# Performance work log

Measured on AMD Instinct MI355X. Metric: run time of the kernel, lower is better.

Reference implementation:

```python
import jax, jax.numpy as jnp
import numpy as np
from jax import lax

T, B = 128, 256          # rollout length x num envs
H, W, C = 7, 7, 3        # minigrid obs
HID = 128                # lstm hidden
NA = 7                   # actions
NFLAT = 64 * 4 * 4       # conv flatten (7->6->5->4)


def setup_inputs() -> dict:
    key = jax.random.key(0)
    ks = jax.random.split(key, 20)
    N = T * B
    obs = jax.random.randint(ks[0], (N, H, W, C), 0, 11).astype(jnp.float32)
    done = (jax.random.uniform(ks[1], (N,)) < 0.05).astype(jnp.float32)
    h0 = jnp.zeros((1, B, HID), jnp.float32)
    c0 = jnp.zeros((1, B, HID), jnp.float32)
    s = 0.1
    conv1_w = jax.random.normal(ks[2], (16, C, 2, 2)) * s
    conv1_b = jnp.zeros((16,), jnp.float32)
    conv2_w = jax.random.normal(ks[3], (32, 16, 2, 2)) * s
    conv2_b = jnp.zeros((32,), jnp.float32)
    conv3_w = jax.random.normal(ks[4], (64, 32, 2, 2)) * s
    conv3_b = jnp.zeros((64,), jnp.float32)
    w_ih = jax.random.normal(ks[5], (4 * HID, NFLAT)) * 0.03
    w_hh = jax.random.normal(ks[6], (4 * HID, HID)) * 0.08
    b_ih = jnp.zeros((4 * HID,), jnp.float32)
    b_hh = jnp.zeros((4 * HID,), jnp.float32)
    actor_w = jax.random.normal(ks[7], (NA, HID)) * 0.01
    actor_b = jnp.zeros((NA,), jnp.float32)
    critic_w = jax.random.normal(ks[8], (1, HID)) * 0.08
    critic_b = jnp.zeros((1,), jnp.float32)
    return dict(obs=obs, done=done, h0=h0, c0=c0,
                conv1_w=conv1_w, conv1_b=conv1_b,
                conv2_w=conv2_w, conv2_b=conv2_b,
                conv3_w=conv3_w, conv3_b=conv3_b,
                w_ih=w_ih, w_hh=w_hh, b_ih=b_ih, b_hh=b_hh,
                actor_w=actor_w, actor_b=actor_b,
                critic_w=critic_w, critic_b=critic_b)


def _conv(x, w, b):
    # x: [N, Cin, h, w], w: [Cout, Cin, 2, 2], VALID, stride 1
    y = lax.conv_general_dilated(x, w, (1, 1), 'VALID',
                                 dimension_numbers=('NCHW', 'OIHW', 'NCHW'))
    return jax.nn.relu(y + b[None, :, None, None])


def reference(obs, done, h0, c0,
              conv1_w, conv1_b, conv2_w, conv2_b, conv3_w, conv3_b,
              w_ih, w_hh, b_ih, b_hh, actor_w, actor_b, critic_w, critic_b):
    N = obs.shape[0]
    x = jnp.transpose(obs, (0, 3, 1, 2))            # NHWC -> NCHW
    x = _conv(x, conv1_w, conv1_b)
    x = _conv(x, conv2_w, conv2_b)
    x = _conv(x, conv3_w, conv3_b)
    feat = x.reshape(N, -1)                          # [T*B, 1024]

    nb = h0.shape[1]
    xs = feat.reshape(-1, nb, feat.shape[-1])        # [T, B, 1024]
    ds = done.reshape(-1, nb)                        # [T, B]
    bias = b_ih + b_hh

    def step(carry, inp):
        h, c = carry                                  # [B, HID]
        x_t, d_t = inp
        m = (1.0 - d_t)[:, None]
        h = m * h
        c = m * c
        gates = x_t @ w_ih.T + h @ w_hh.T + bias      # [B, 4*HID]
        i, f, g, o = jnp.split(gates, 4, axis=-1)     # torch gate order i,f,g,o
        i = jax.nn.sigmoid(i)
        f = jax.nn.sigmoid(f)
        g = jnp.tanh(g)
        o = jax.nn.sigmoid(o)
        c = f * c + i * g
        h = o * jnp.tanh(c)
        return (h, c), h

    (hT, cT), hs = lax.scan(step, (h0[0], c0[0]), (xs, ds))
    hid = hs.reshape(N, -1)                           # [T*B, HID]
    logits = hid @ actor_w.T + actor_b                # [T*B, NA]
    value = hid @ critic_w.T + critic_b               # [T*B, 1]
    out = jnp.concatenate([logits, value], axis=-1)   # [T*B, NA+1]
    return out, hT[None], cT[None]
```

## Files before the change

kernel.cpp:

```cpp
#include <hip/hip_runtime.h>
#include <hip/hip_bf16.h>


#define N_IMG   32768
#define T_LEN   128
#define B_ENV   256
#define HID     128

typedef _Float16 f16x8 __attribute__((ext_vector_type(8)));
typedef _Float16 f16x2 __attribute__((ext_vector_type(2)));
typedef float    f32x4 __attribute__((ext_vector_type(4)));
typedef unsigned short ushort8v __attribute__((ext_vector_type(8)));
typedef unsigned short ushort4v __attribute__((ext_vector_type(4)));

#if defined(__has_builtin)
#if __has_builtin(__builtin_amdgcn_exp2f)
#define FEXP2(x) __builtin_amdgcn_exp2f(x)
#endif
#if __has_builtin(__builtin_amdgcn_rcpf)
#define FRCP(x) __builtin_amdgcn_rcpf(x)
#endif
#endif
#ifndef FEXP2
#define FEXP2(x) exp2f(x)
#endif
#ifndef FRCP
#define FRCP(x) (1.0f / (x))
#endif

__device__ __forceinline__ float sigm_(float x) {
    return FRCP(1.0f + FEXP2(-1.44269504f * x));
}
__device__ __forceinline__ float tanh_(float x) {
    return fmaf(-2.0f, FRCP(1.0f + FEXP2(2.88539008f * x)), 1.0f);
}

__device__ __forceinline__ unsigned short f2h(float x) {
    _Float16 h = (_Float16)x;
    union { _Float16 h; unsigned short u; } un; un.h = h;
    return un.u;
}

#if defined(__has_builtin)
#if __has_builtin(__builtin_amdgcn_fdot2)
#define HAVE_FDOT2 1
#endif
#endif

__device__ __forceinline__ float dot2_(f16x2 a, f16x2 b, float c) {
#ifdef HAVE_FDOT2
    return __builtin_amdgcn_fdot2(a, b, c, false);
#else
    c = fmaf((float)a[0], (float)b[0], c);
    return fmaf((float)a[1], (float)b[1], c);
#endif
}

#define P0(v) __builtin_shufflevector(v, v, 0, 1)
#define P1(v) __builtin_shufflevector(v, v, 2, 3)
#define P2(v) __builtin_shufflevector(v, v, 4, 5)
#define P3(v) __builtin_shufflevector(v, v, 6, 7)

__device__ __forceinline__ float bfly_sum4(float x) {
    int y = __builtin_amdgcn_update_dpp(0, __float_as_int(x), 0xB1, 0xF, 0xF, true);
    x += __int_as_float(y);
    y = __builtin_amdgcn_update_dpp(0, __float_as_int(x), 0x4E, 0xF, 0xF, true);
    return x + __int_as_float(y);
}

#define GLDS16(g, l) __builtin_amdgcn_global_load_lds( \
    (const __attribute__((address_space(1))) unsigned int*)(g), \
    (__attribute__((address_space(3))) unsigned int*)(l), 16, 0, 0)

__global__ void prep_all(const float* __restrict__ w_ih, unsigned short* __restrict__ wb,
                         const float* __restrict__ w2, const float* __restrict__ w3,
                         unsigned short* __restrict__ wb2g, unsigned short* __restrict__ wb3g,
                         const float* __restrict__ w_hh, unsigned short* __restrict__ whhr)
{
    const int bid = blockIdx.x, tid = threadIdx.x;
    if (bid < 2048) {
        const int idx = bid * 256 + tid;
        const int np = idx >> 10, kk = idx & 1023;
        const int p = kk >> 6, co = kk & 63;
        const int g = np & 3, ci = np >> 2;
        wb[idx] = f2h(w_ih[(g * 128 + ci) * 1024 + co * 16 + p]);
    } else if (bid < 2088) {
        const int t = (bid - 2048) * 256 + tid;
        if (t < 2048) {
            const int j = t & 7, lane = (t >> 3) & 63, f = t >> 9;
            const int ky = f >> 1, ct = f & 1;
            const int k = ((lane >> 4) << 3) + j, kx = k >> 4, ci = k & 15;
            wb2g[t] = f2h(w2[(ct * 16 + (lane & 15)) * 64 + ci * 4 + ky * 2 + kx]);
        } else {
            const int u = t - 2048;
            const int j = u & 7, lane = (u >> 3) & 63, f = u >> 9;
            const int ct = f >> 2, pos = f & 3;
            const int ci = ((lane >> 4) << 3) + j;
            wb3g[u] = f2h(w3[(ct * 16 + (lane & 15)) * 128 + ci * 4 + pos]);
        }
    } else {
        const int idx = (bid - 2088) * 256 + tid;
        const int thr = idx >> 7, r = idx & 127;
        const int g = r >> 5, k = r & 31;
        const int ci = thr >> 2, s = thr & 3;
        whhr[idx] = f2h(w_hh[(g * 128 + ci) * 128 + s * 32 + k]);
    }
}

__global__ __launch_bounds__(256, 2) void conv_fused(
    const float* __restrict__ obs,
    const float* __restrict__ w1, const float* __restrict__ b1,
    const float* __restrict__ b2, const float* __restrict__ b3,
    const unsigned short* __restrict__ wb2g,
    const unsigned short* __restrict__ wb3g,
    unsigned short* __restrict__ featb)
{
    __shared__ __align__(16) unsigned char u1[25856];
    __shared__ __align__(16) unsigned char u2[33024];
    __shared__ float w1s[192];
    __shared__ float b1s[16];

    float* s_obs = (float*)u1;
    unsigned short* c2s = (unsigned short*)u1;
    unsigned short* c1s = (unsigned short*)u2;
    unsigned short* c3s = (unsigned short*)u2;

    const int tid = threadIdx.x, lane = tid & 63, wv = tid >> 6;
    const int base = blockIdx.x * 16;

    if (tid < 192) w1s[tid] = w1[tid];
    if (tid < 16)  b1s[tid] = b1[tid];
    for (int i = tid; i < 16 * 147; i += 256) {
        const int im = i / 147, r = i - im * 147;
        s_obs[im * 148 + r] = obs[(size_t)(base + im) * 147 + r];
    }
    __syncthreads();

    {
        const int img = tid & 15;
        const float* ob = &s_obs[img * 148];
        for (int p = tid >> 4; p < 36; p += 16) {
            const int py = p / 6, px = p % 6;
            float o[12];
#pragma unroll
            for (int ky = 0; ky < 2; ky++)
#pragma unroll
                for (int kx = 0; kx < 2; kx++)
#pragma unroll
                    for (int cc = 0; cc < 3; cc++)
                        o[cc * 4 + ky * 2 + kx] = ob[((py + ky) * 7 + px + kx) * 3 + cc];
            unsigned short res[16];
#pragma unroll
            for (int ci = 0; ci < 16; ci++) {
                float a = b1s[ci];
#pragma unroll
                for (int q = 0; q < 12; q++) a = fmaf(o[q], w1s[ci * 12 + q], a);
                res[ci] = f2h(fmaxf(a, 0.0f));
            }
            *(ushort8v*)&c1s[img * 584 + p * 16]     = *(ushort8v*)&res[0];
            *(ushort8v*)&c1s[img * 584 + p * 16 + 8] = *(ushort8v*)&res[8];
        }
    }
    __syncthreads();

    {
        const int ct = wv & 1, par = wv >> 1;
        const int img = lane & 15, kq = lane >> 4;
        f16x8 wA[2];
        wA[0] = *(const f16x8*)&wb2g[(0 + ct) * 512 + lane * 8];
        wA[1] = *(const f16x8*)&wb2g[(2 + ct) * 512 + lane * 8];
        const float4 b2v = *(const float4*)&b2[ct * 16 + kq * 4];
#pragma unroll 2
        for (int p = par; p < 25; p += 2) {
            const int py = p / 5, px = p % 5;
            f32x4 acc = {0.f, 0.f, 0.f, 0.f};
#pragma unroll
            for (int ky = 0; ky < 2; ky++) {
                const int pix = (py + ky) * 6 + px + (kq >> 1);
                const f16x8 bv = *(const f16x8*)&c1s[img * 584 + pix * 16 + (kq & 1) * 8];
                acc = __builtin_amdgcn_mfma_f32_16x16x32_f16(wA[ky], bv, acc, 0, 0, 0);
            }
            unsigned short r4[4];
            r4[0] = f2h(fmaxf(acc[0] + b2v.x, 0.0f));
            r4[1] = f2h(fmaxf(acc[1] + b2v.y, 0.0f));
            r4[2] = f2h(fmaxf(acc[2] + b2v.z, 0.0f));
            r4[3] = f2h(fmaxf(acc[3] + b2v.w, 0.0f));
            *(ushort4v*)&c2s[img * 808 + p * 32 + ct * 16 + kq * 4] = *(ushort4v*)&r4[0];
        }
    }
    __syncthreads();

    {
        const int ct = wv;
        const int img = lane & 15, kq = lane >> 4;
        f16x8 wA3[4];
#pragma unroll
        for (int pos = 0; pos < 4; pos++)
            wA3[pos] = *(const f16x8*)&wb3g[(ct * 4 + pos) * 512 + lane * 8];
        const float4 b3v = *(const float4*)&b3[ct * 16 + kq * 4];
#pragma unroll 4
        for (int p = 0; p < 16; p++) {
            const int py = p >> 2, px = p & 3;
            f32x4 acc = {0.f, 0.f, 0.f, 0.f};
#pragma unroll
            for (int pos = 0; pos < 4; pos++) {
                const int pix = (py + (pos >> 1)) * 5 + px + (pos & 1);
                const f16x8 bv = *(const f16x8*)&c2s[img * 808 + pix * 32 + kq * 8];
                acc = __builtin_amdgcn_mfma_f32_16x16x32_f16(wA3[pos], bv, acc, 0, 0, 0);
            }
            unsigned short r4[4];
            r4[0] = f2h(fmaxf(acc[0] + b3v.x, 0.0f));
            r4[1] = f2h(fmaxf(acc[1] + b3v.y, 0.0f));
            r4[2] = f2h(fmaxf(acc[2] + b3v.z, 0.0f));
            r4[3] = f2h(fmaxf(acc[3] + b3v.w, 0.0f));
            *(ushort4v*)&c3s[img * 1032 + p * 64 + ct * 16 + kq * 4] = *(ushort4v*)&r4[0];
        }
    }
    __syncthreads();

#pragma unroll
    for (int i = 0; i < 8; i++) {
        const int gi = i * 2048 + tid * 8;
        const int img = gi >> 10, flat = gi & 1023;
        *(ushort8v*)&featb[(size_t)(base + img) * 1024 + flat] =
            *(const ushort8v*)&c3s[img * 1032 + flat];
    }
}

__global__ __launch_bounds__(256, 2) void gemm_xproj_mfma(
    const unsigned short* __restrict__ A,
    const unsigned short* __restrict__ W,
    float* __restrict__ C)
{
    __shared__ unsigned short As[2][128 * 32];
    __shared__ unsigned short Bs[2][128 * 32];

    const int tid  = threadIdx.x;
    const int wg = (blockIdx.x & 7) * 128 + (blockIdx.x >> 3);
    const int bx = wg & 3;
    const int by = wg >> 2;
    const int m0 = by * 128, n0 = bx * 128;
    const int lane = tid & 63, wave = tid >> 6;
    const int wm = (wave >> 1) * 64, wn = (wave & 1) * 64;
    const int srow = tid >> 2, sseg = tid & 3;

    const unsigned short* Ag = A + (size_t)(m0 + srow) * 1024 + sseg * 8;
    const unsigned short* Wg = W + (size_t)(n0 + srow) * 1024 + sseg * 8;

    f32x4 acc[4][4];
#pragma unroll
    for (int i = 0; i < 4; i++)
#pragma unroll
        for (int j = 0; j < 4; j++) acc[i][j] = (f32x4){0.f, 0.f, 0.f, 0.f};

    const int fr = lane & 15, fq = lane >> 4;

#define STAGEK(bb, k0) do {                                                \
        GLDS16(Ag + (k0),             (char*)&As[bb][0] + tid * 16);       \
        GLDS16(Ag + (k0) + 64 * 1024, (char*)&As[bb][0] + tid * 16 + 4096);\
        GLDS16(Wg + (k0),             (char*)&Bs[bb][0] + tid * 16);       \
        GLDS16(Wg + (k0) + 64 * 1024, (char*)&Bs[bb][0] + tid * 16 + 4096);\
    } while (0)

    STAGEK(0, 0);
    asm volatile("s_waitcnt vmcnt(0)" ::: "memory");
    __syncthreads();

    int cur = 0;
    for (int ks = 0; ks < 32; ks++) {
        if (ks + 1 < 32) STAGEK(cur ^ 1, (ks + 1) * 32);

        f16x8 af[4], bfv[4];
#pragma unroll
        for (int i = 0; i < 4; i++)
            af[i] = *(const f16x8*)&As[cur][(wm + i * 16 + fr) * 32 + fq * 8];
#pragma unroll
        for (int j = 0; j < 4; j++)
            bfv[j] = *(const f16x8*)&Bs[cur][(wn + j * 16 + fr) * 32 + fq * 8];
#pragma unroll
        for (int i = 0; i < 4; i++)
#pragma unroll
            for (int j = 0; j < 4; j++)
                acc[i][j] = __builtin_amdgcn_mfma_f32_16x16x32_f16(af[i], bfv[j], acc[i][j], 0, 0, 0);

        asm volatile("s_waitcnt vmcnt(0)" ::: "memory");
        __syncthreads();
        cur ^= 1;
    }
#undef STAGEK

    const int cr = fq * 4, cc = fr;
#pragma unroll
    for (int i = 0; i < 4; i++) {
#pragma unroll
        for (int j = 0; j < 4; j++) {
            float* cp = &C[(size_t)(m0 + wm + i * 16 + cr) * 512 + (n0 + wn + j * 16 + cc)];
#pragma unroll
            for (int r = 0; r < 4; r++)
                cp[(size_t)r * 512] = acc[i][j][r];
        }
    }
}

__global__ __launch_bounds__(512) __attribute__((amdgpu_waves_per_eu(2, 2)))
void lstm_bfly(
    const float* __restrict__ xproj, const float* __restrict__ done,
    const float* __restrict__ h0, const float* __restrict__ c0,
    const unsigned short* __restrict__ whhr,
    const float* __restrict__ b_ih, const float* __restrict__ b_hh,
    unsigned short* __restrict__ hid16, float* __restrict__ out)
{
    const int b   = blockIdx.x;
    const int tid = threadIdx.x;
    const int ci  = tid >> 2;
    const int s   = tid & 3;

    __shared__ __align__(16) _Float16 hbuf[2][HID];

    f16x8 w[4][4];
    {
        const unsigned short* wp = whhr + (size_t)tid * 128;
#pragma unroll
        for (int g = 0; g < 4; g++)
#pragma unroll
            for (int i = 0; i < 4; i++)
                w[g][i] = *(const f16x8*)&wp[g * 32 + i * 8];
    }
    const float bias_l = b_ih[s * 128 + ci] + b_hh[s * 128 + ci];

    float c = c0[b * HID + ci];
    float h = h0[b * HID + ci];
    float dcur = done[b];

    if (tid < HID)
        hbuf[0][tid] = (_Float16)(h0[b * HID + tid] * (1.0f - dcur));

    float xq = bias_l + xproj[(size_t)b * 512 + ci * 4 + s];
    __syncthreads();

#define DOTBLK(i, c0_, c1_, c2_, c3_)                                           \
    {                                                                           \
        const f16x8 hv8 = *(const f16x8*)&hbuf[p][s * 32 + (i) * 8];            \
        const f16x2 hp0 = P0(hv8), hp1 = P1(hv8), hp2 = P2(hv8), hp3 = P3(hv8); \
        c0_ = dot2_(P0(w[0][i]), hp0, c0_); c0_ = dot2_(P1(w[0][i]), hp1, c0_); \
        c0_ = dot2_(P2(w[0][i]), hp2, c0_); c0_ = dot2_(P3(w[0][i]), hp3, c0_); \
        c1_ = dot2_(P0(w[1][i]), hp0, c1_); c1_ = dot2_(P1(w[1][i]), hp1, c1_); \
        c1_ = dot2_(P2(w[1][i]), hp2, c1_); c1_ = dot2_(P3(w[1][i]), hp3, c1_); \
        c2_ = dot2_(P0(w[2][i]), hp0, c2_); c2_ = dot2_(P1(w[2][i]), hp1, c2_); \
        c2_ = dot2_(P2(w[2][i]), hp2, c2_); c2_ = dot2_(P3(w[2][i]), hp3, c2_); \
        c3_ = dot2_(P0(w[3][i]), hp0, c3_); c3_ = dot2_(P1(w[3][i]), hp1, c3_); \
        c3_ = dot2_(P2(w[3][i]), hp2, c3_); c3_ = dot2_(P3(w[3][i]), hp3, c3_); \
    }

    int p = 0;
    for (int t = 0; t < T_LEN; t++) {
        const int tn = (t + 1 < T_LEN) ? t + 1 : t;
        const float xqn = bias_l + xproj[((size_t)tn * B_ENV + b) * 512 + ci * 4 + s];
        const float dnn = done[tn * B_ENV + b];

        float a0 = (s == 0) ? xq : 0.0f;
        float a1 = (s == 1) ? xq : 0.0f;
        float a2 = (s == 2) ? xq : 0.0f;
        float a3 = (s == 3) ? xq : 0.0f;
        float b0 = 0.f, b1 = 0.f, b2 = 0.f, b3 = 0.f;
        DOTBLK(0, a0, a1, a2, a3)
        DOTBLK(1, b0, b1, b2, b3)
        DOTBLK(2, a0, a1, a2, a3)
        DOTBLK(3, b0, b1, b2, b3)
        a0 += b0; a1 += b1; a2 += b2; a3 += b3;

        a0 = bfly_sum4(a0); a1 = bfly_sum4(a1);
        a2 = bfly_sum4(a2); a3 = bfly_sum4(a3);

        const float gi = sigm_(a0), gf = sigm_(a1);
        const float gg = tanh_(a2), go = sigm_(a3);
        const float m = 1.0f - dcur;
        c = fmaf(gf, c * m, gi * gg);
        h = go * tanh_(c);

        if (s == 0) {
            hid16[((size_t)t * B_ENV + b) * HID + ci] = f2h(h);
            hbuf[p ^ 1][ci] = (_Float16)(h * (1.0f - dnn));
        }

        xq = xqn; dcur = dnn; p ^= 1;
        __syncthreads();
    }

    if (s == 0) {
        out[262144 + b * HID + ci] = h;
        out[294912 + b * HID + ci] = c;
    }
#undef DOTBLK
}

__global__ __launch_bounds__(256, 2) void heads_kernel(
    const unsigned short* __restrict__ hid16,
    const float* __restrict__ aw, const float* __restrict__ ab,
    const float* __restrict__ cw, const float* __restrict__ cb,
    float* __restrict__ out)
{
    __shared__ float hs[32 * 129];
    __shared__ float ws[8 * 130];
    __shared__ float bs[8];

    const int tid = threadIdx.x;
    const int n0 = blockIdx.x * 32;

    for (int i = tid; i < 1024; i += 256) {
        const int r = i >> 7, k = i & 127;
        ws[r * 130 + k] = (r < 7) ? aw[r * 128 + k] : cw[k];
    }
    if (tid < 8) bs[tid] = (tid < 7) ? ab[tid] : cb[0];
    for (int i = tid; i < 512; i += 256) {
        const int r = i >> 4, k8 = (i & 15) * 8;
        const ushort8v v = *(const ushort8v*)&hid16[(size_t)(n0 + r) * 128 + k8];
#pragma unroll
        for (int q = 0; q < 8; q++) {
            union { unsigned short u; _Float16 h; } un; un.u = v[q];
            hs[r * 129 + k8 + q] = (float)un.h;
        }
    }
    __syncthreads();

    const int r = tid >> 3, jj = tid & 7;
    float acc = bs[jj];
    const float* hp = &hs[r * 129];
    const float* wp = &ws[jj * 130];
#pragma unroll
    for (int k = 0; k < 128; k++) acc = fmaf(hp[k], wp[k], acc);
    out[(size_t)(n0 + r) * 8 + jj] = acc;
}

extern "C" void kernel_launch(void* const* d_in, const int* in_sizes, int n_in,
                              void* d_out, int out_size, void* d_ws, size_t ws_size,
                              hipStream_t stream)
{
    (void)in_sizes; (void)n_in; (void)out_size; (void)ws_size;

    const float* obs  = (const float*)d_in[0];
    const float* done = (const float*)d_in[1];
    const float* h0   = (const float*)d_in[2];
    const float* c0   = (const float*)d_in[3];
    const float* w1   = (const float*)d_in[4];
    const float* b1   = (const float*)d_in[5];
    const float* w2   = (const float*)d_in[6];
    const float* b2   = (const float*)d_in[7];
    const float* w3   = (const float*)d_in[8];
    const float* b3   = (const float*)d_in[9];
    const float* w_ih = (const float*)d_in[10];
    const float* w_hh = (const float*)d_in[11];
    const float* b_ih = (const float*)d_in[12];
    const float* b_hh = (const float*)d_in[13];
    const float* aw   = (const float*)d_in[14];
    const float* ab   = (const float*)d_in[15];
    const float* cw   = (const float*)d_in[16];
    const float* cb   = (const float*)d_in[17];
    float* out = (float*)d_out;

    unsigned short* featb = (unsigned short*)d_ws;
    unsigned short* wb    = featb + 33554432ull;
    unsigned short* wb2g  = wb    + 524288ull;
    unsigned short* wb3g  = wb2g  + 2048ull;
    float* xproj = (float*)(wb3g + 8192ull + 2048ull);
    unsigned short* hid16 = (unsigned short*)(xproj + 16777216ull);
    unsigned short* whhr  = hid16 + 4194304ull;

    prep_all<<<2344, 256, 0, stream>>>(w_ih, wb, w2, w3, wb2g, wb3g, w_hh, whhr);
    conv_fused<<<2048, 256, 0, stream>>>(obs, w1, b1, b2, b3, wb2g, wb3g, featb);
    gemm_xproj_mfma<<<1024, 256, 0, stream>>>(featb, wb, xproj);
    lstm_bfly<<<256, 512, 0, stream>>>(xproj, done, h0, c0, whhr, b_ih, b_hh, hid16, out);
    heads_kernel<<<1024, 256, 0, stream>>>(hid16, aw, ab, cw, cb, out);
}
```

Baseline: 270.0 us.

## Fold weight prep into conv kernel and enlarge xproj GEMM tile to 256x128

```diff
diff --git a/kernel.cpp b/kernel.cpp
--- a/kernel.cpp
+++ b/kernel.cpp
@@ -72,47 +72,13 @@
     (const __attribute__((address_space(1))) unsigned int*)(g), \
     (__attribute__((address_space(3))) unsigned int*)(l), 16, 0, 0)
 
-__global__ void prep_all(const float* __restrict__ w_ih, unsigned short* __restrict__ wb,
-                         const float* __restrict__ w2, const float* __restrict__ w3,
-                         unsigned short* __restrict__ wb2g, unsigned short* __restrict__ wb3g,
-                         const float* __restrict__ w_hh, unsigned short* __restrict__ whhr)
-{
-    const int bid = blockIdx.x, tid = threadIdx.x;
-    if (bid < 2048) {
-        const int idx = bid * 256 + tid;
-        const int np = idx >> 10, kk = idx & 1023;
-        const int p = kk >> 6, co = kk & 63;
-        const int g = np & 3, ci = np >> 2;
-        wb[idx] = f2h(w_ih[(g * 128 + ci) * 1024 + co * 16 + p]);
-    } else if (bid < 2088) {
-        const int t = (bid - 2048) * 256 + tid;
-        if (t < 2048) {
-            const int j = t & 7, lane = (t >> 3) & 63, f = t >> 9;
-            const int ky = f >> 1, ct = f & 1;
-            const int k = ((lane >> 4) << 3) + j, kx = k >> 4, ci = k & 15;
-            wb2g[t] = f2h(w2[(ct * 16 + (lane & 15)) * 64 + ci * 4 + ky * 2 + kx]);
-        } else {
-            const int u = t - 2048;
-            const int j = u & 7, lane = (u >> 3) & 63, f = u >> 9;
-            const int ct = f >> 2, pos = f & 3;
-            const int ci = ((lane >> 4) << 3) + j;
-            wb3g[u] = f2h(w3[(ct * 16 + (lane & 15)) * 128 + ci * 4 + pos]);
-        }
-    } else {
-        const int idx = (bid - 2088) * 256 + tid;
-        const int thr = idx >> 7, r = idx & 127;
-        const int g = r >> 5, k = r & 31;
-        const int ci = thr >> 2, s = thr & 3;
-        whhr[idx] = f2h(w_hh[(g * 128 + ci) * 128 + s * 32 + k]);
-    }
-}
-
 __global__ __launch_bounds__(256, 2) void conv_fused(
     const float* __restrict__ obs,
     const float* __restrict__ w1, const float* __restrict__ b1,
-    const float* __restrict__ b2, const float* __restrict__ b3,
-    const unsigned short* __restrict__ wb2g,
-    const unsigned short* __restrict__ wb3g,
+    const float* __restrict__ w2, const float* __restrict__ b2,
+    const float* __restrict__ w3, const float* __restrict__ b3,
+    const float* __restrict__ w_ih, unsigned short* __restrict__ wbout,
+    const float* __restrict__ w_hh, unsigned short* __restrict__ whhrout,
     unsigned short* __restrict__ featb)
 {
     __shared__ __align__(16) unsigned char u1[25856];
@@ -128,6 +94,19 @@
     const int tid = threadIdx.x, lane = tid & 63, wv = tid >> 6;
     const int base = blockIdx.x * 16;
 
+    {
+        const int idx = blockIdx.x * 256 + tid;
+        const int np = idx >> 10, kk = idx & 1023;
+        const int p = kk >> 6, co = kk & 63;
+        const int g = np & 3, ci = np >> 2;
+        wbout[idx] = f2h(w_ih[(g * 128 + ci) * 1024 + co * 16 + p]);
+        if (blockIdx.x < 256) {
+            const int thr = idx >> 7, r = idx & 127;
+            whhrout[idx] = f2h(w_hh[((r >> 5) * 128 + (thr >> 2)) * 128 +
+                                    (thr & 3) * 32 + (r & 31)]);
+        }
+    }
+
     if (tid < 192) w1s[tid] = w1[tid];
     if (tid < 16)  b1s[tid] = b1[tid];
     for (int i = tid; i < 16 * 147; i += 256) {
@@ -167,8 +146,18 @@
         const int ct = wv & 1, par = wv >> 1;
         const int img = lane & 15, kq = lane >> 4;
         f16x8 wA[2];
-        wA[0] = *(const f16x8*)&wb2g[(0 + ct) * 512 + lane * 8];
-        wA[1] = *(const f16x8*)&wb2g[(2 + ct) * 512 + lane * 8];
+        {
+            const float* w2b = w2 + (ct * 16 + (lane & 15)) * 64;
+            const int cib = (kq & 1) * 8, kx = kq >> 1;
+#pragma unroll
+            for (int ky = 0; ky < 2; ky++) {
+                float t[8];
+#pragma unroll
+                for (int j = 0; j < 8; j++) t[j] = w2b[(cib + j) * 4 + ky * 2 + kx];
+                wA[ky] = (f16x8){(_Float16)t[0], (_Float16)t[1], (_Float16)t[2], (_Float16)t[3],
+                                 (_Float16)t[4], (_Float16)t[5], (_Float16)t[6], (_Float16)t[7]};
+            }
+        }
         const float4 b2v = *(const float4*)&b2[ct * 16 + kq * 4];
 #pragma unroll 2
         for (int p = par; p < 25; p += 2) {
@@ -194,9 +183,17 @@
         const int ct = wv;
         const int img = lane & 15, kq = lane >> 4;
         f16x8 wA3[4];
-#pragma unroll
-        for (int pos = 0; pos < 4; pos++)
-            wA3[pos] = *(const f16x8*)&wb3g[(ct * 4 + pos) * 512 + lane * 8];
+        {
+            const float* w3b = w3 + (ct * 16 + (lane & 15)) * 128;
+#pragma unroll
+            for (int pos = 0; pos < 4; pos++) {
+                float t[8];
+#pragma unroll
+                for (int j = 0; j < 8; j++) t[j] = w3b[(kq * 8 + j) * 4 + pos];
+                wA3[pos] = (f16x8){(_Float16)t[0], (_Float16)t[1], (_Float16)t[2], (_Float16)t[3],
+                                   (_Float16)t[4], (_Float16)t[5], (_Float16)t[6], (_Float16)t[7]};
+            }
+        }
         const float4 b3v = *(const float4*)&b3[ct * 16 + kq * 4];
 #pragma unroll 4
         for (int p = 0; p < 16; p++) {
@@ -227,25 +224,28 @@
     }
 }
 
-__global__ __launch_bounds__(256, 2) void gemm_xproj_mfma(
+__global__ __launch_bounds__(512) __attribute__((amdgpu_waves_per_eu(4, 4)))
+void gemm_xproj_mfma(
     const unsigned short* __restrict__ A,
     const unsigned short* __restrict__ W,
     float* __restrict__ C)
 {
-    __shared__ unsigned short As[2][128 * 32];
+    __shared__ unsigned short As[2][256 * 32];
     __shared__ unsigned short Bs[2][128 * 32];
 
     const int tid  = threadIdx.x;
-    const int wg = (blockIdx.x & 7) * 128 + (blockIdx.x >> 3);
+    const int wg = (blockIdx.x & 7) * 64 + (blockIdx.x >> 3);
     const int bx = wg & 3;
     const int by = wg >> 2;
-    const int m0 = by * 128, n0 = bx * 128;
+    const int m0 = by * 256, n0 = bx * 128;
     const int lane = tid & 63, wave = tid >> 6;
-    const int wm = (wave >> 1) * 64, wn = (wave & 1) * 64;
+    const int wm = (wave >> 1) * 64;
+    const int wn = (wave & 1) * 64;
     const int srow = tid >> 2, sseg = tid & 3;
 
-    const unsigned short* Ag = A + (size_t)(m0 + srow) * 1024 + sseg * 8;
-    const unsigned short* Wg = W + (size_t)(n0 + srow) * 1024 + sseg * 8;
+    const unsigned short* Ag  = A + (size_t)(m0 + srow) * 1024 + sseg * 8;
+    const unsigned short* Ag2 = Ag + 128 * 1024;
+    const unsigned short* Wg  = W + (size_t)(n0 + srow) * 1024 + sseg * 8;
 
     f32x4 acc[4][4];
 #pragma unroll
@@ -255,11 +255,10 @@
 
     const int fr = lane & 15, fq = lane >> 4;
 
-#define STAGEK(bb, k0) do {                                                \
-        GLDS16(Ag + (k0),             (char*)&As[bb][0] + tid * 16);       \
-        GLDS16(Ag + (k0) + 64 * 1024, (char*)&As[bb][0] + tid * 16 + 4096);\
-        GLDS16(Wg + (k0),             (char*)&Bs[bb][0] + tid * 16);       \
-        GLDS16(Wg + (k0) + 64 * 1024, (char*)&Bs[bb][0] + tid * 16 + 4096);\
+#define STAGEK(bb, k0) do {                                                 \
+        GLDS16(Ag  + (k0), (char*)&As[bb][0] + tid * 16);                   \
+        GLDS16(Ag2 + (k0), (char*)&As[bb][0] + tid * 16 + 8192);            \
+        GLDS16(Wg  + (k0), (char*)&Bs[bb][0] + tid * 16);                   \
     } while (0)
 
     STAGEK(0, 0);
@@ -466,9 +465,9 @@
     unsigned short* hid16 = (unsigned short*)(xproj + 16777216ull);
     unsigned short* whhr  = hid16 + 4194304ull;
 
-    prep_all<<<2344, 256, 0, stream>>>(w_ih, wb, w2, w3, wb2g, wb3g, w_hh, whhr);
-    conv_fused<<<2048, 256, 0, stream>>>(obs, w1, b1, b2, b3, wb2g, wb3g, featb);
-    gemm_xproj_mfma<<<1024, 256, 0, stream>>>(featb, wb, xproj);
+    conv_fused<<<2048, 256, 0, stream>>>(obs, w1, b1, w2, b2, w3, b3,
+                                         w_ih, wb, w_hh, whhr, featb);
+    gemm_xproj_mfma<<<512, 512, 0, stream>>>(featb, wb, xproj);
     lstm_bfly<<<256, 512, 0, stream>>>(xproj, done, h0, c0, whhr, b_ih, b_hh, hid16, out);
     heads_kernel<<<1024, 256, 0, stream>>>(hid16, aw, ab, cw, cb, out);
 }
```

Result: slower. 282.3 us (+4.6%).

## Use MFMA for LSTM recurrent matvec with LDS gate exchange

Applied to the files above, without the earlier changes.

```diff
diff --git a/kernel.cpp b/kernel.cpp
--- a/kernel.cpp
+++ b/kernel.cpp
@@ -39,33 +39,6 @@
     _Float16 h = (_Float16)x;
     union { _Float16 h; unsigned short u; } un; un.h = h;
     return un.u;
-}
-
-#if defined(__has_builtin)
-#if __has_builtin(__builtin_amdgcn_fdot2)
-#define HAVE_FDOT2 1
-#endif
-#endif
-
-__device__ __forceinline__ float dot2_(f16x2 a, f16x2 b, float c) {
-#ifdef HAVE_FDOT2
-    return __builtin_amdgcn_fdot2(a, b, c, false);
-#else
-    c = fmaf((float)a[0], (float)b[0], c);
-    return fmaf((float)a[1], (float)b[1], c);
-#endif
-}
-
-#define P0(v) __builtin_shufflevector(v, v, 0, 1)
-#define P1(v) __builtin_shufflevector(v, v, 2, 3)
-#define P2(v) __builtin_shufflevector(v, v, 4, 5)
-#define P3(v) __builtin_shufflevector(v, v, 6, 7)
-
-__device__ __forceinline__ float bfly_sum4(float x) {
-    int y = __builtin_amdgcn_update_dpp(0, __float_as_int(x), 0xB1, 0xF, 0xF, true);
-    x += __int_as_float(y);
-    y = __builtin_amdgcn_update_dpp(0, __float_as_int(x), 0x4E, 0xF, 0xF, true);
-    return x + __int_as_float(y);
 }
 
 #define GLDS16(g, l) __builtin_amdgcn_global_load_lds( \
@@ -100,10 +73,11 @@
         }
     } else {
         const int idx = (bid - 2088) * 256 + tid;
-        const int thr = idx >> 7, r = idx & 127;
-        const int g = r >> 5, k = r & 31;
-        const int ci = thr >> 2, s = thr & 3;
-        whhr[idx] = f2h(w_hh[(g * 128 + ci) * 128 + s * 32 + k]);
+        const int j = idx & 7, lane = (idx >> 3) & 63, f = idx >> 9;
+        const int kk = f & 3, t4 = (f >> 2) & 3, wv = f >> 4;
+        const int row = t4 * 128 + wv * 16 + (lane & 15);
+        const int col = kk * 32 + ((lane >> 4) << 3) + j;
+        whhr[idx] = f2h(w_hh[row * 128 + col]);
     }
 }
 
@@ -303,77 +277,83 @@
 }
 
 __global__ __launch_bounds__(512) __attribute__((amdgpu_waves_per_eu(2, 2)))
-void lstm_bfly(
+void lstm_mfma(
     const float* __restrict__ xproj, const float* __restrict__ done,
     const float* __restrict__ h0, const float* __restrict__ c0,
     const unsigned short* __restrict__ whhr,
     const float* __restrict__ b_ih, const float* __restrict__ b_hh,
     unsigned short* __restrict__ hid16, float* __restrict__ out)
 {
-    const int b   = blockIdx.x;
-    const int tid = threadIdx.x;
-    const int ci  = tid >> 2;
-    const int s   = tid & 3;
+    const int b    = blockIdx.x;
+    const int tid  = threadIdx.x;
+    const int lane = tid & 63, wv = tid >> 6;
+    const int fr   = lane & 15, q = lane >> 4;
+    const int ci   = tid >> 2;
+    const int s    = tid & 3;
 
     __shared__ __align__(16) _Float16 hbuf[2][HID];
-
-    f16x8 w[4][4];
-    {
-        const unsigned short* wp = whhr + (size_t)tid * 128;
-#pragma unroll
-        for (int g = 0; g < 4; g++)
-#pragma unroll
-            for (int i = 0; i < 4; i++)
-                w[g][i] = *(const f16x8*)&wp[g * 32 + i * 8];
-    }
-    const float bias_l = b_ih[s * 128 + ci] + b_hh[s * 128 + ci];
+    __shared__ __align__(16) float gate_lds[HID * 4];
+
+    f16x8 af[4][4];
+#pragma unroll
+    for (int t4 = 0; t4 < 4; t4++)
+#pragma unroll
+        for (int kk = 0; kk < 4; kk++)
+            af[t4][kk] = *(const f16x8*)&whhr[(size_t)(((wv * 4 + t4) * 4 + kk) * 64 + lane) * 8];
+
+    float bias4[4];
+#pragma unroll
+    for (int g = 0; g < 4; g++)
+        bias4[g] = b_ih[g * 128 + ci] + b_hh[g * 128 + ci];
 
     float c = c0[b * HID + ci];
-    float h = h0[b * HID + ci];
+    float h = 0.0f;
     float dcur = done[b];
-
     if (tid < HID)
         hbuf[0][tid] = (_Float16)(h0[b * HID + tid] * (1.0f - dcur));
 
-    float xq = bias_l + xproj[(size_t)b * 512 + ci * 4 + s];
-    __syncthreads();
-
-#define DOTBLK(i, c0_, c1_, c2_, c3_)                                           \
-    {                                                                           \
-        const f16x8 hv8 = *(const f16x8*)&hbuf[p][s * 32 + (i) * 8];            \
-        const f16x2 hp0 = P0(hv8), hp1 = P1(hv8), hp2 = P2(hv8), hp3 = P3(hv8); \
-        c0_ = dot2_(P0(w[0][i]), hp0, c0_); c0_ = dot2_(P1(w[0][i]), hp1, c0_); \
-        c0_ = dot2_(P2(w[0][i]), hp2, c0_); c0_ = dot2_(P3(w[0][i]), hp3, c0_); \
-        c1_ = dot2_(P0(w[1][i]), hp0, c1_); c1_ = dot2_(P1(w[1][i]), hp1, c1_); \
-        c1_ = dot2_(P2(w[1][i]), hp2, c1_); c1_ = dot2_(P3(w[1][i]), hp3, c1_); \
-        c2_ = dot2_(P0(w[2][i]), hp0, c2_); c2_ = dot2_(P1(w[2][i]), hp1, c2_); \
-        c2_ = dot2_(P2(w[2][i]), hp2, c2_); c2_ = dot2_(P3(w[2][i]), hp3, c2_); \
-        c3_ = dot2_(P0(w[3][i]), hp0, c3_); c3_ = dot2_(P1(w[3][i]), hp1, c3_); \
-        c3_ = dot2_(P2(w[3][i]), hp2, c3_); c3_ = dot2_(P3(w[3][i]), hp3, c3_); \
-    }
+    float xpb[4];
+    {
+        const float4 v = *(const float4*)&xproj[(size_t)b * 512 + ci * 4];
+        xpb[0] = v.x + bias4[0]; xpb[1] = v.y + bias4[1];
+        xpb[2] = v.z + bias4[2]; xpb[3] = v.w + bias4[3];
+    }
+    __syncthreads();
 
     int p = 0;
     for (int t = 0; t < T_LEN; t++) {
         const int tn = (t + 1 < T_LEN) ? t + 1 : t;
-        const float xqn = bias_l + xproj[((size_t)tn * B_ENV + b) * 512 + ci * 4 + s];
+        const float4 nv = *(const float4*)&xproj[((size_t)tn * B_ENV + b) * 512 + ci * 4];
         const float dnn = done[tn * B_ENV + b];
 
-        float a0 = (s == 0) ? xq : 0.0f;
-        float a1 = (s == 1) ? xq : 0.0f;
-        float a2 = (s == 2) ? xq : 0.0f;
-        float a3 = (s == 3) ? xq : 0.0f;
-        float b0 = 0.f, b1 = 0.f, b2 = 0.f, b3 = 0.f;
-        DOTBLK(0, a0, a1, a2, a3)
-        DOTBLK(1, b0, b1, b2, b3)
-        DOTBLK(2, a0, a1, a2, a3)
-        DOTBLK(3, b0, b1, b2, b3)
-        a0 += b0; a1 += b1; a2 += b2; a3 += b3;
-
-        a0 = bfly_sum4(a0); a1 = bfly_sum4(a1);
-        a2 = bfly_sum4(a2); a3 = bfly_sum4(a3);
-
-        const float gi = sigm_(a0), gf = sigm_(a1);
-        const float gg = tanh_(a2), go = sigm_(a3);
+        f16x8 bf[4];
+#pragma unroll
+        for (int kk = 0; kk < 4; kk++)
+            bf[kk] = *(const f16x8*)&hbuf[p][kk * 32 + q * 8];
+
+        f32x4 acc[4];
+#pragma unroll
+        for (int t4 = 0; t4 < 4; t4++) acc[t4] = (f32x4){0.f, 0.f, 0.f, 0.f};
+#pragma unroll
+        for (int kk = 0; kk < 4; kk++)
+#pragma unroll
+            for (int t4 = 0; t4 < 4; t4++)
+                acc[t4] = __builtin_amdgcn_mfma_f32_16x16x32_f16(af[t4][kk], bf[kk], acc[t4], 0, 0, 0);
+
+        if (fr == 0) {
+#pragma unroll
+            for (int t4 = 0; t4 < 4; t4++)
+#pragma unroll
+                for (int r = 0; r < 4; r++)
+                    gate_lds[(wv * 16 + q * 4 + r) * 4 + t4] = acc[t4][r];
+        }
+        __syncthreads();
+
+        const float4 g4 = *(const float4*)&gate_lds[ci * 4];
+        const float gi = sigm_(g4.x + xpb[0]);
+        const float gf = sigm_(g4.y + xpb[1]);
+        const float gg = tanh_(g4.z + xpb[2]);
+        const float go = sigm_(g4.w + xpb[3]);
         const float m = 1.0f - dcur;
         c = fmaf(gf, c * m, gi * gg);
         h = go * tanh_(c);
@@ -383,7 +363,9 @@
             hbuf[p ^ 1][ci] = (_Float16)(h * (1.0f - dnn));
         }
 
-        xq = xqn; dcur = dnn; p ^= 1;
+        xpb[0] = nv.x + bias4[0]; xpb[1] = nv.y + bias4[1];
+        xpb[2] = nv.z + bias4[2]; xpb[3] = nv.w + bias4[3];
+        dcur = dnn; p ^= 1;
         __syncthreads();
     }
 
@@ -391,7 +373,6 @@
         out[262144 + b * HID + ci] = h;
         out[294912 + b * HID + ci] = c;
     }
-#undef DOTBLK
 }
 
 __global__ __launch_bounds__(256, 2) void heads_kernel(
@@ -469,6 +450,6 @@
     prep_all<<<2344, 256, 0, stream>>>(w_ih, wb, w2, w3, wb2g, wb3g, w_hh, whhr);
     conv_fused<<<2048, 256, 0, stream>>>(obs, w1, b1, b2, b3, wb2g, wb3g, featb);
     gemm_xproj_mfma<<<1024, 256, 0, stream>>>(featb, wb, xproj);
-    lstm_bfly<<<256, 512, 0, stream>>>(xproj, done, h0, c0, whhr, b_ih, b_hh, hid16, out);
+    lstm_mfma<<<256, 512, 0, stream>>>(xproj, done, h0, c0, whhr, b_ih, b_hh, hid16, out);
     heads_kernel<<<1024, 256, 0, stream>>>(hid16, aw, ab, cw, cb, out);
 }
```

Result: slower. 307.1 us (+13.7%).
